# Optimization experiments

Hardware: AMD Instinct MI355X
Metric: run time of the kernel (lower is better)

Reference implementation:

```python
import jax, jax.numpy as jnp
import numpy as np
from jax import lax

STRIDE = (1, 1)
PADDING = ((1, 1), (1, 1))
DILATION = (1, 1)


def setup_inputs() -> dict:
    key = jax.random.key(0)
    k1, k2, k3, k4 = jax.random.split(key, 4)
    B, FIN, FOUT, K, H, W = 32, 256, 256, 3, 56, 56
    x = jax.random.normal(k1, (B, FIN, H, W), dtype=jnp.float32)
    m = jax.random.uniform(k2, (B, FOUT, FIN, K, K), dtype=jnp.float32)  # dynamic per-sample mask
    weight = jax.random.normal(k3, (FOUT, FIN, K, K), dtype=jnp.float32) * 0.05
    bias = jax.random.normal(k4, (FOUT,), dtype=jnp.float32) * 0.05
    return {"x": x, "m": m, "weight": weight, "bias": bias}


def _conv_one(xi, wi):
    # xi: [fin, H, W], wi: [fout, fin, kh, kw] -> [fout, H', W']
    out = lax.conv_general_dilated(
        xi[None], wi,
        window_strides=STRIDE,
        padding=PADDING,
        rhs_dilation=DILATION,
        dimension_numbers=("NCHW", "OIHW", "NCHW"),
    )
    return out[0]


def reference(x, m, weight, bias):
    # Per-sample masked weights: [B, fout, fin, kh, kw]
    mask_weight = weight[None] * m
    # vmap over batch: each sample uses its own conv kernel (the groups=B trick)
    out = jax.vmap(_conv_one)(x, mask_weight)  # [B, fout, H', W']
    return out + bias[None, :, None, None]
```

## Files before the change

kernel.cpp:

```cpp
#include <hip/hip_runtime.h>
#include <hip/hip_bf16.h>

typedef __attribute__((ext_vector_type(8))) short short8;
typedef __attribute__((ext_vector_type(4))) short short4v;
typedef __attribute__((ext_vector_type(4))) float f32x4;

#define BATCH 32
#define NCH   256
#define HW    56
#define NPIX  3136
#define XT_R  58

#define XT_SLAB   (XT_R * XT_R * 32 * 2)
#define XT_BYTES  ((size_t)BATCH * 8 * XT_SLAB)
#define WM_TAP    (256 * 32 * 2)
#define WM_SLAB   (9 * WM_TAP)
#define WM_B      (8 * WM_SLAB)
#define WM_BYTES  ((size_t)BATCH * WM_B)
#define WS_NEEDED (XT_BYTES + WM_BYTES)

#define GLL16(g, l) __builtin_amdgcn_global_load_lds( \
    (const __attribute__((address_space(1))) void*)(g), \
    (__attribute__((address_space(3))) void*)(l), 16, 0, 0)

static __device__ __forceinline__ short f2bf(float f) {
    union { __hip_bfloat16 h; short s; } u;
    u.h = __float2bfloat16(f);
    return u.s;
}

__global__ __launch_bounds__(256) void halo_zero(char* xtb) {
    const int t = threadIdx.x;
    unsigned* p = (unsigned*)(xtb + (size_t)blockIdx.x * XT_SLAB);
    for (int i = t; i < 928; i += 256) { p[i] = 0u; p[57 * 928 + i] = 0u; }
    for (int j = t; j < 896; j += 256) {
        int r = (j >> 4) + 1, c = j & 15;
        p[r * 928 + c] = 0u;
        p[r * 928 + 912 + c] = 0u;
    }
}

__global__ __launch_bounds__(256) void wm_prep(const float* __restrict__ w,
                                               const float* __restrict__ m,
                                               char* __restrict__ wmb) {
    __shared__ short prod[2304];
    const int b = blockIdx.x >> 8, fo = blockIdx.x & 255, t = threadIdx.x;
    const float4* m4 = (const float4*)(m + ((size_t)(b * NCH + fo)) * 2304);
    const float4* w4 = (const float4*)(w + (size_t)fo * 2304);
#pragma unroll
    for (int i = 0; i < 3; ++i) {
        int idx = i * 256 + t;
        if (idx < 576) {
            float4 a = w4[idx], mm = m4[idx];
            short4v s;
            s.x = f2bf(a.x * mm.x); s.y = f2bf(a.y * mm.y);
            s.z = f2bf(a.z * mm.z); s.w = f2bf(a.w * mm.w);
            ((short4v*)prod)[idx] = s;
        }
    }
    __syncthreads();
    char* ob = wmb + (size_t)b * WM_B + fo * 64;
#pragma unroll
    for (int i = 0; i < 5; ++i) {
        int q = i * 256 + t;
        if (q < 1152) {
            int o = q * 2;
            int s = o / 288, r = o - s * 288;
            int tap = r >> 5, fi = r & 31;
            unsigned lo = (unsigned short)prod[(s * 32 + fi) * 9 + tap];
            unsigned hi = (unsigned short)prod[(s * 32 + fi + 1) * 9 + tap];
            *(unsigned*)(ob + s * WM_SLAB + tap * WM_TAP + fi * 2) = lo | (hi << 16);
        }
    }
}

__global__ __launch_bounds__(256) void xt_prep(const float* __restrict__ x,
                                               char* __restrict__ xtb) {
    __shared__ short xl[NCH * HW];
    const int blk = blockIdx.x;
    const int b = blk / HW, h = blk % HW, t = threadIdx.x;
    const float4* x4 = (const float4*)(x + (size_t)b * NCH * NPIX);
    const int rowb = h * 14;
#pragma unroll
    for (int i = 0; i < 14; ++i) {
        int c = i * 256 + t;
        int fi = c / 14, j = c - fi * 14;
        float4 v = x4[(size_t)fi * 784 + rowb + j];
        short4v s;
        s.x = f2bf(v.x); s.y = f2bf(v.y); s.z = f2bf(v.z); s.w = f2bf(v.w);
        ((short4v*)xl)[fi * 14 + j] = s;
    }
    __syncthreads();
    char* ob = xtb + (size_t)(b * 8) * XT_SLAB + (h + 1) * 3712 + 64;
#pragma unroll
    for (int i = 0; i < 28; ++i) {
        int q = i * 256 + t;
        int s = q / 896, rr = q - s * 896;
        int ww = rr >> 4, fp = rr & 15;
        int fi = s * 32 + 2 * fp;
        unsigned lo = (unsigned short)xl[fi * HW + ww];
        unsigned hi = (unsigned short)xl[(fi + 1) * HW + ww];
        *(unsigned*)(ob + s * XT_SLAB + ww * 64 + fp * 4) = lo | (hi << 16);
    }
}

__global__ __launch_bounds__(256, 2) void gemm_dwa(const char* __restrict__ xtb,
                                                   const char* __restrict__ wmb,
                                                   const float* __restrict__ bias,
                                                   float* __restrict__ out) {
    __shared__ short Alds[2304 * 8];
    __shared__ short Blds[2560 * 8];

    const int tid = threadIdx.x, lane = tid & 63, wv = tid >> 6;
    const int ln = lane & 15, kg = lane >> 4;

    const int blk = blockIdx.x;
    const int xcd = blk & 7, slot = blk >> 3;
    const int b = xcd + 8 * (slot / 28);
    const int inner = slot % 28;
    const int ft = inner / 7, rt = inner % 7;
    const int fo0 = ft * 64, h0 = rt * 8;

    int pbase[7];
#pragma unroll
    for (int ni = 0; ni < 7; ++ni) {
        int p = wv * 112 + ni * 16 + ln;
        int hh = p / 56;
        pbase[ni] = hh * XT_R + (p - hh * 56);
    }

    const char* Ag = wmb + (size_t)b * WM_B + fo0 * 64;
    const char* Bg = xtb + (size_t)(b * 8) * XT_SLAB + h0 * 3712;

    f32x4 acc[4][7];
#pragma unroll
    for (int mi = 0; mi < 4; ++mi)
#pragma unroll
        for (int ni = 0; ni < 7; ++ni) acc[mi][ni] = (f32x4)0.0f;

    for (int s = 0; s < 8; ++s) {
        const char* ag = Ag + s * WM_SLAB;
        const char* bg = Bg + (size_t)s * XT_SLAB;

        __syncthreads();
#pragma unroll
        for (int i = 0; i < 9; ++i) {
            int c = i * 256 + tid;
            GLL16(ag + (c >> 8) * WM_TAP + (c & 255) * 16,
                  (char*)Alds + (i * 256 + wv * 64) * 16);
        }
#pragma unroll
        for (int i = 0; i < 10; ++i) {
            int c = i * 256 + tid;
            GLL16(bg + c * 16,
                  (char*)Blds + (i * 256 + wv * 64) * 16);
        }
        __syncthreads();

#pragma unroll
        for (int tap = 0; tap < 9; ++tap) {
            const int kh = tap / 3, kw = tap - kh * 3;
            const int shift = (kh * XT_R + kw) * 64;
            short8 af[4];
#pragma unroll
            for (int mi = 0; mi < 4; ++mi)
                af[mi] = *(const short8*)((const char*)Alds + tap * 4096 + (mi * 16 + ln) * 64 + kg * 16);
            short8 bf[7];
#pragma unroll
            for (int ni = 0; ni < 7; ++ni)
                bf[ni] = *(const short8*)((const char*)Blds + pbase[ni] * 64 + shift + kg * 16);
#pragma unroll
            for (int mi = 0; mi < 4; ++mi)
#pragma unroll
                for (int ni = 0; ni < 7; ++ni)
                    acc[mi][ni] = __builtin_amdgcn_mfma_f32_16x16x32_bf16(
                        af[mi], bf[ni], acc[mi][ni], 0, 0, 0);
        }
    }

#pragma unroll
    for (int mi = 0; mi < 4; ++mi) {
#pragma unroll
        for (int r = 0; r < 4; ++r) {
            const int row = fo0 + mi * 16 + kg * 4 + r;
            const float bv = bias[row];
            float* op = out + ((size_t)(b * NCH + row)) * NPIX + rt * 448 + wv * 112;
#pragma unroll
            for (int ni = 0; ni < 7; ++ni)
                op[ni * 16 + ln] = acc[mi][ni][r] + bv;
        }
    }
}

#define XS_W 60
#define XS_H 58
#define NGROUPS (NPIX / 4)
__global__ __launch_bounds__(256) void conv_dwa_fp32(
    const float* __restrict__ x, const float* __restrict__ m,
    const float* __restrict__ weight, const float* __restrict__ bias,
    float* __restrict__ out) {
    __shared__ float xs[XS_H * XS_W];
    const int tid = threadIdx.x, blk = blockIdx.x;
    const int b = blk >> 8, fo = blk & 255;
    const float* xb = x + (size_t)b * NCH * NPIX;
    const float* mb = m + ((size_t)b * NCH + fo) * (NCH * 9);
    const float* wb = weight + (size_t)fo * (NCH * 9);
    float acc[4][4];
#pragma unroll
    for (int g = 0; g < 4; ++g)
#pragma unroll
        for (int i = 0; i < 4; ++i) acc[g][i] = 0.0f;
    int rowbase[4];
#pragma unroll
    for (int g = 0; g < 4; ++g) {
        int p0 = (tid + g * 256) * 4;
        int gh = p0 / HW;
        rowbase[g] = gh * XS_W + (p0 - gh * HW);
    }
    for (int fi = 0; fi < NCH; ++fi) {
        const float* xp = xb + (size_t)fi * NPIX;
        __syncthreads();
        for (int idx = tid; idx < XS_H * 58; idx += 256) {
            int hh = idx / 58, ww = idx - hh * 58;
            int h = hh - 1, w = ww - 1;
            float v = 0.0f;
            if ((unsigned)h < HW && (unsigned)w < HW) v = xp[h * HW + w];
            xs[hh * XS_W + ww] = v;
        }
        float wm9[9];
#pragma unroll
        for (int j = 0; j < 9; ++j) wm9[j] = wb[fi * 9 + j] * mb[fi * 9 + j];
        __syncthreads();
#pragma unroll
        for (int g = 0; g < 4; ++g) {
            if (tid + g * 256 >= NGROUPS) break;
            const float* row0 = &xs[rowbase[g]];
#pragma unroll
            for (int kh = 0; kh < 3; ++kh) {
                const float* r = row0 + kh * XS_W;
                float s0 = r[0], s1 = r[1], s2 = r[2], s3 = r[3], s4 = r[4], s5 = r[5];
                const float w0 = wm9[3 * kh], w1 = wm9[3 * kh + 1], w2 = wm9[3 * kh + 2];
                acc[g][0] = fmaf(s2, w2, fmaf(s1, w1, fmaf(s0, w0, acc[g][0])));
                acc[g][1] = fmaf(s3, w2, fmaf(s2, w1, fmaf(s1, w0, acc[g][1])));
                acc[g][2] = fmaf(s4, w2, fmaf(s3, w1, fmaf(s2, w0, acc[g][2])));
                acc[g][3] = fmaf(s5, w2, fmaf(s4, w1, fmaf(s3, w0, acc[g][3])));
            }
        }
    }
    const float bv = bias[fo];
    float* ob = out + ((size_t)b * NCH + fo) * NPIX;
#pragma unroll
    for (int g = 0; g < 4; ++g) {
        int gi = tid + g * 256;
        if (gi >= NGROUPS) break;
        float4 v;
        v.x = acc[g][0] + bv; v.y = acc[g][1] + bv;
        v.z = acc[g][2] + bv; v.w = acc[g][3] + bv;
        *(float4*)(ob + gi * 4) = v;
    }
}

extern "C" void kernel_launch(void* const* d_in, const int* in_sizes, int n_in,
                              void* d_out, int out_size, void* d_ws, size_t ws_size,
                              hipStream_t stream) {
    const float* x      = (const float*)d_in[0];
    const float* m      = (const float*)d_in[1];
    const float* weight = (const float*)d_in[2];
    const float* bias   = (const float*)d_in[3];
    float* out          = (float*)d_out;

    if (ws_size < WS_NEEDED) {
        conv_dwa_fp32<<<dim3(BATCH * NCH), dim3(256), 0, stream>>>(x, m, weight, bias, out);
        return;
    }

    char* xtb = (char*)d_ws;
    char* wmb = xtb + XT_BYTES;

    halo_zero<<<dim3(BATCH * 8), dim3(256), 0, stream>>>(xtb);
    wm_prep<<<dim3(BATCH * NCH), dim3(256), 0, stream>>>(weight, m, wmb);
    xt_prep<<<dim3(BATCH * HW), dim3(256), 0, stream>>>(x, xtb);
    gemm_dwa<<<dim3(896), dim3(256), 0, stream>>>(xtb, wmb, bias, out);
}
```

Before: 357.4 us.

## Merge prep kernels into one launch with swizzled LDS and 16-byte stores

```diff
diff --git a/kernel.cpp b/kernel.cpp
--- a/kernel.cpp
+++ b/kernel.cpp
@@ -4,6 +4,7 @@
 typedef __attribute__((ext_vector_type(8))) short short8;
 typedef __attribute__((ext_vector_type(4))) short short4v;
 typedef __attribute__((ext_vector_type(4))) float f32x4;
+typedef __attribute__((ext_vector_type(4))) int i32x4;
 
 #define BATCH 32
 #define NCH   256
@@ -19,6 +20,11 @@
 #define WM_BYTES  ((size_t)BATCH * WM_B)
 #define WS_NEEDED (XT_BYTES + WM_BYTES)
 
+#define XT_BLKS   (BATCH * HW)
+#define WM_BLKS   (BATCH * NCH)
+#define HALO_BLKS (BATCH * 8)
+#define PREP_BLKS (XT_BLKS + WM_BLKS + HALO_BLKS)
+
 #define GLL16(g, l) __builtin_amdgcn_global_load_lds( \
     (const __attribute__((address_space(1))) void*)(g), \
     (__attribute__((address_space(3))) void*)(l), 16, 0, 0)
@@ -29,78 +35,87 @@
     return u.s;
 }
 
-__global__ __launch_bounds__(256) void halo_zero(char* xtb) {
+__global__ __launch_bounds__(256) void prep_all(const float* __restrict__ x,
+                                                const float* __restrict__ w,
+                                                const float* __restrict__ m,
+                                                char* __restrict__ xtb,
+                                                char* __restrict__ wmb) {
+    __shared__ __align__(16) char lds[28672];
     const int t = threadIdx.x;
-    unsigned* p = (unsigned*)(xtb + (size_t)blockIdx.x * XT_SLAB);
-    for (int i = t; i < 928; i += 256) { p[i] = 0u; p[57 * 928 + i] = 0u; }
-    for (int j = t; j < 896; j += 256) {
-        int r = (j >> 4) + 1, c = j & 15;
-        p[r * 928 + c] = 0u;
-        p[r * 928 + 912 + c] = 0u;
-    }
-}
-
-__global__ __launch_bounds__(256) void wm_prep(const float* __restrict__ w,
-                                               const float* __restrict__ m,
-                                               char* __restrict__ wmb) {
-    __shared__ short prod[2304];
-    const int b = blockIdx.x >> 8, fo = blockIdx.x & 255, t = threadIdx.x;
-    const float4* m4 = (const float4*)(m + ((size_t)(b * NCH + fo)) * 2304);
-    const float4* w4 = (const float4*)(w + (size_t)fo * 2304);
-#pragma unroll
-    for (int i = 0; i < 3; ++i) {
-        int idx = i * 256 + t;
-        if (idx < 576) {
-            float4 a = w4[idx], mm = m4[idx];
-            short4v s;
-            s.x = f2bf(a.x * mm.x); s.y = f2bf(a.y * mm.y);
-            s.z = f2bf(a.z * mm.z); s.w = f2bf(a.w * mm.w);
-            ((short4v*)prod)[idx] = s;
-        }
-    }
-    __syncthreads();
-    char* ob = wmb + (size_t)b * WM_B + fo * 64;
-#pragma unroll
-    for (int i = 0; i < 5; ++i) {
-        int q = i * 256 + t;
-        if (q < 1152) {
-            int o = q * 2;
-            int s = o / 288, r = o - s * 288;
-            int tap = r >> 5, fi = r & 31;
-            unsigned lo = (unsigned short)prod[(s * 32 + fi) * 9 + tap];
-            unsigned hi = (unsigned short)prod[(s * 32 + fi + 1) * 9 + tap];
-            *(unsigned*)(ob + s * WM_SLAB + tap * WM_TAP + fi * 2) = lo | (hi << 16);
-        }
-    }
-}
-
-__global__ __launch_bounds__(256) void xt_prep(const float* __restrict__ x,
-                                               char* __restrict__ xtb) {
-    __shared__ short xl[NCH * HW];
     const int blk = blockIdx.x;
-    const int b = blk / HW, h = blk % HW, t = threadIdx.x;
-    const float4* x4 = (const float4*)(x + (size_t)b * NCH * NPIX);
-    const int rowb = h * 14;
-#pragma unroll
-    for (int i = 0; i < 14; ++i) {
-        int c = i * 256 + t;
-        int fi = c / 14, j = c - fi * 14;
-        float4 v = x4[(size_t)fi * 784 + rowb + j];
-        short4v s;
-        s.x = f2bf(v.x); s.y = f2bf(v.y); s.z = f2bf(v.z); s.w = f2bf(v.w);
-        ((short4v*)xl)[fi * 14 + j] = s;
-    }
-    __syncthreads();
-    char* ob = xtb + (size_t)(b * 8) * XT_SLAB + (h + 1) * 3712 + 64;
-#pragma unroll
-    for (int i = 0; i < 28; ++i) {
-        int q = i * 256 + t;
-        int s = q / 896, rr = q - s * 896;
-        int ww = rr >> 4, fp = rr & 15;
-        int fi = s * 32 + 2 * fp;
-        unsigned lo = (unsigned short)xl[fi * HW + ww];
-        unsigned hi = (unsigned short)xl[(fi + 1) * HW + ww];
-        *(unsigned*)(ob + s * XT_SLAB + ww * 64 + fp * 4) = lo | (hi << 16);
+
+    if (blk < XT_BLKS) {
+        unsigned* xl2 = (unsigned*)lds;
+        const int b = blk / HW, h = blk % HW;
+        const float4* x4 = (const float4*)(x + (size_t)b * NCH * NPIX);
+        const int rowb = h * 14;
+#pragma unroll
+        for (int it = 0; it < 7; ++it) {
+            int c = it * 256 + t;
+            int p = c / 14, j = c - p * 14;
+            float4 a  = x4[(size_t)(2 * p)     * 784 + rowb + j];
+            float4 bb = x4[(size_t)(2 * p + 1) * 784 + rowb + j];
+            int col = p ^ ((j & 7) << 2);
+            unsigned d0 = ((unsigned)(unsigned short)f2bf(a.x)) | (((unsigned)(unsigned short)f2bf(bb.x)) << 16);
+            unsigned d1 = ((unsigned)(unsigned short)f2bf(a.y)) | (((unsigned)(unsigned short)f2bf(bb.y)) << 16);
+            unsigned d2 = ((unsigned)(unsigned short)f2bf(a.z)) | (((unsigned)(unsigned short)f2bf(bb.z)) << 16);
+            unsigned d3 = ((unsigned)(unsigned short)f2bf(a.w)) | (((unsigned)(unsigned short)f2bf(bb.w)) << 16);
+            unsigned* base = xl2 + j * 512 + col;
+            base[0]   = d0;
+            base[128] = d1;
+            base[256] = d2;
+            base[384] = d3;
+        }
+        __syncthreads();
+        char* ob = xtb + (size_t)(b * 8) * XT_SLAB + (h + 1) * 3712 + 64;
+#pragma unroll
+        for (int it = 0; it < 7; ++it) {
+            int c = it * 256 + t;
+            int s = c / 224, rem = c - s * 224;
+            int ww = rem >> 2, u = rem & 3;
+            int col = (s * 16 + u * 4) ^ (((ww >> 2) & 7) << 2);
+            i32x4 v = *(const i32x4*)(xl2 + ww * 128 + col);
+            *(i32x4*)(ob + (size_t)s * XT_SLAB + ww * 64 + u * 16) = v;
+        }
+    } else if (blk < XT_BLKS + WM_BLKS) {
+        short* prod2 = (short*)lds;
+        const int bk = blk - XT_BLKS;
+        const int b = bk >> 8, fo = bk & 255;
+        const float4* m4 = (const float4*)(m + ((size_t)(b * NCH + fo)) * 2304);
+        const float4* w4 = (const float4*)(w + (size_t)fo * 2304);
+#pragma unroll
+        for (int i = 0; i < 3; ++i) {
+            int idx = i * 256 + t;
+            if (idx < 576) {
+                float4 a = w4[idx], mm = m4[idx];
+                int flat = idx * 4;
+                float pr[4];
+                pr[0] = a.x * mm.x; pr[1] = a.y * mm.y;
+                pr[2] = a.z * mm.z; pr[3] = a.w * mm.w;
+#pragma unroll
+                for (int k2 = 0; k2 < 4; ++k2) {
+                    int f2 = flat + k2;
+                    int fi = f2 / 9, tap = f2 - fi * 9;
+                    *(short*)((char*)prod2 + tap * 512 + ((fi * 2) ^ ((tap & 3) << 4))) = f2bf(pr[k2]);
+                }
+            }
+        }
+        __syncthreads();
+        char* ob = wmb + (size_t)b * WM_B + fo * 64;
+        for (int q = t; q < 288; q += 256) {
+            int s = q / 36, r = q - s * 36;
+            int tap = r >> 2, u = r & 3;
+            i32x4 v = *(const i32x4*)((char*)prod2 + tap * 512 + ((s * 64 + u * 16) ^ ((tap & 3) << 4)));
+            *(i32x4*)(ob + (size_t)s * WM_SLAB + tap * WM_TAP + u * 16) = v;
+        }
+    } else {
+        unsigned* p = (unsigned*)(xtb + (size_t)(blk - XT_BLKS - WM_BLKS) * XT_SLAB);
+        for (int i = t; i < 928; i += 256) { p[i] = 0u; p[57 * 928 + i] = 0u; }
+        for (int j = t; j < 896; j += 256) {
+            int r = (j >> 4) + 1, c = j & 15;
+            p[r * 928 + c] = 0u;
+            p[r * 928 + 912 + c] = 0u;
+        }
     }
 }
 
@@ -277,8 +292,6 @@
     char* xtb = (char*)d_ws;
     char* wmb = xtb + XT_BYTES;
 
-    halo_zero<<<dim3(BATCH * 8), dim3(256), 0, stream>>>(xtb);
-    wm_prep<<<dim3(BATCH * NCH), dim3(256), 0, stream>>>(weight, m, wmb);
-    xt_prep<<<dim3(BATCH * HW), dim3(256), 0, stream>>>(x, xtb);
+    prep_all<<<dim3(PREP_BLKS), dim3(256), 0, stream>>>(x, weight, m, xtb, wmb);
     gemm_dwa<<<dim3(896), dim3(256), 0, stream>>>(xtb, wmb, bias, out);
 }
```

Result: faster. 338.0 us (-5.4%).
